# Optimization experiments

Measured on AMD Instinct MI355X. Metric: run time of the kernel, lower is better.

Reference implementation:

```python
import jax, jax.numpy as jnp
import numpy as np

HEADS = 8

def setup_inputs() -> dict:
    key = jax.random.key(0)
    ks = jax.random.split(key, 5)
    B, C, H, W = 2, 256, 64, 64
    dim = C
    x = jax.random.normal(ks[0], (B, C, H, W), dtype=jnp.float32)
    # Linear weights stored as [in, out] so y = x @ W + b
    w_qkv = jax.random.normal(ks[1], (dim, 3 * dim), dtype=jnp.float32) * (dim ** -0.5)
    b_qkv = jax.random.normal(ks[2], (3 * dim,), dtype=jnp.float32) * 0.02
    w_out = jax.random.normal(ks[3], (dim, dim), dtype=jnp.float32) * (dim ** -0.5)
    b_out = jax.random.normal(ks[4], (dim,), dtype=jnp.float32) * 0.02
    return {"x": x, "w_qkv": w_qkv, "b_qkv": b_qkv, "w_out": w_out, "b_out": b_out}

def reference(x, w_qkv, b_qkv, w_out, b_out):
    B, C, H, W = x.shape
    h = HEADS
    d = C // h
    scale = d ** -0.5
    # [B, C, H, W] -> [B, N, C]
    tokens = x.reshape(B, C, H * W).transpose(0, 2, 1)
    qkv = tokens @ w_qkv + b_qkv  # [B, N, 3C]
    q, k, v = jnp.split(qkv, 3, axis=-1)
    def to_heads(t):
        Bn, N, _ = t.shape
        return t.reshape(Bn, N, h, d).transpose(0, 2, 1, 3)  # [B, h, N, d]
    q, k, v = map(to_heads, (q, k, v))
    dots = jnp.einsum('bhnd,bhmd->bhnm', q, k) * scale  # [B, h, N, N]
    attn = jax.nn.softmax(dots, axis=-1)
    out = jnp.einsum('bhnm,bhmd->bhnd', attn, v)  # [B, h, N, d]
    out = out.transpose(0, 2, 1, 3).reshape(B, H * W, C)  # [B, N, C]
    out = out @ w_out + b_out
    return out.transpose(0, 2, 1).reshape(B, C, H, W)
```

## Files before the change

kernel.cpp:

```cpp
#include <hip/hip_runtime.h>

typedef __attribute__((ext_vector_type(8))) short s16x8;
typedef __attribute__((ext_vector_type(4))) short s16x4;
typedef __attribute__((ext_vector_type(4))) float f32x4;
typedef __attribute__((ext_vector_type(2))) unsigned u32x2;

#define MFMA32(a, b, c) __builtin_amdgcn_mfma_f32_16x16x32_bf16((a), (b), (c), 0, 0, 0)

#if __has_builtin(__builtin_amdgcn_mfma_f32_16x16x16bf16_1k)
#define MFMA16K(a, b, c) __builtin_amdgcn_mfma_f32_16x16x16bf16_1k((a), (b), (c), 0, 0, 0)
#else
#define MFMA16K(a, b, c) (c)
#endif

#if __has_builtin(__builtin_amdgcn_exp2f)
#define EXP2F(x) __builtin_amdgcn_exp2f(x)
#else
#define EXP2F(x) __exp2f(x)
#endif

#if __has_builtin(__builtin_amdgcn_rcpf)
#define RCPF(x) __builtin_amdgcn_rcpf(x)
#else
#define RCPF(x) (1.0f / (x))
#endif

#define SL2E 0.25507313f

__device__ __forceinline__ unsigned pkrne(float a, float b) {
  unsigned ua = __builtin_bit_cast(unsigned, a);
  unsigned ub = __builtin_bit_cast(unsigned, b);
  ua += 0x7FFFu + ((ua >> 16) & 1u);
  ub += 0x7FFFu + ((ub >> 16) & 1u);
  return __builtin_amdgcn_perm(ub, ua, 0x07060302u);
}

__device__ __forceinline__ unsigned pktrunc(float a, float b) {
  return __builtin_amdgcn_perm(__builtin_bit_cast(unsigned, b),
                               __builtin_bit_cast(unsigned, a), 0x07060302u);
}

__device__ __forceinline__ unsigned short bfr(float f) {
  unsigned u = __builtin_bit_cast(unsigned, f);
  u += 0x7FFFu + ((u >> 16) & 1u);
  return (unsigned short)(u >> 16);
}

__global__ __launch_bounds__(256) void prep_kernel(
    const float* __restrict__ x, const float* __restrict__ wqkv,
    const float* __restrict__ wout, ushort* __restrict__ xbf,
    ushort* __restrict__ wT, ushort* __restrict__ woT) {
  const int t = threadIdx.x;
  const int sub = t & 15, grp = t >> 4;
  const int id = blockIdx.x;
  const float* src;
  ushort* dst;
  int src_ld, k0, n0;
  float sc = 1.f;
  if (id < 512) {
    int mt = id & 63, kt = (id >> 6) & 3, b = id >> 8;
    src = x + (size_t)b * 256 * 4096;
    src_ld = 4096;
    dst = xbf + (size_t)b * 4096 * 256;
    k0 = kt * 64;
    n0 = mt * 64;
  } else if (id < 560) {
    int r = id - 512, nt = r % 12, kt = r / 12;
    src = wqkv;
    src_ld = 768;
    dst = wT;
    k0 = kt * 64;
    n0 = nt * 64;
    if (n0 < 256) sc = SL2E;
  } else {
    int r = id - 560, nt = r & 3, kt = r >> 2;
    src = wout;
    src_ld = 256;
    dst = woT;
    k0 = kt * 64;
    n0 = nt * 64;
  }
  const int k = k0 + grp * 4;
  const int n = n0 + sub * 4;
  unsigned d0[4], d1[4];
#pragma unroll
  for (int i = 0; i < 4; ++i) {
    float4 v = *(const float4*)(src + (size_t)(k + i) * src_ld + n);
    d0[i] = pkrne(v.x * sc, v.y * sc);
    d1[i] = pkrne(v.z * sc, v.w * sc);
  }
  u32x2 r0 = {__builtin_amdgcn_perm(d0[1], d0[0], 0x05040100u),
              __builtin_amdgcn_perm(d0[3], d0[2], 0x05040100u)};
  u32x2 r1 = {__builtin_amdgcn_perm(d0[1], d0[0], 0x07060302u),
              __builtin_amdgcn_perm(d0[3], d0[2], 0x07060302u)};
  u32x2 r2 = {__builtin_amdgcn_perm(d1[1], d1[0], 0x05040100u),
              __builtin_amdgcn_perm(d1[3], d1[2], 0x05040100u)};
  u32x2 r3 = {__builtin_amdgcn_perm(d1[1], d1[0], 0x07060302u),
              __builtin_amdgcn_perm(d1[3], d1[2], 0x07060302u)};
  *(u32x2*)(dst + (size_t)(n + 0) * 256 + k) = r0;
  *(u32x2*)(dst + (size_t)(n + 1) * 256 + k) = r1;
  *(u32x2*)(dst + (size_t)(n + 2) * 256 + k) = r2;
  *(u32x2*)(dst + (size_t)(n + 3) * 256 + k) = r3;
}

__global__ __launch_bounds__(256) void qkv_kernel(
    const ushort* __restrict__ xbf, const ushort* __restrict__ wT,
    const float* __restrict__ bq, ushort* __restrict__ QG,
    ushort* __restrict__ KG, ushort* __restrict__ VtG) {
  __shared__ __align__(16) ushort Wl[64][40];
  __shared__ __align__(16) ushort Xl[128][40];
  const int t0 = blockIdx.x * 128;
  const int n0 = blockIdx.y * 64;
  const int t = threadIdx.x;
  const int wid = t >> 6, lane = t & 63;
  const int wy = wid >> 1, wx = wid & 1;
  const int quad = lane >> 4, l16 = lane & 15;
  f32x4 acc[2][4] = {};
  const int wr = t >> 2, wsg = t & 3;
  for (int k0 = 0; k0 < 256; k0 += 32) {
    __syncthreads();
    *(uint4*)&Wl[wr][wsg * 8] =
        *(const uint4*)(wT + (size_t)(n0 + wr) * 256 + k0 + wsg * 8);
#pragma unroll
    for (int i = 0; i < 2; ++i) {
      int fid = t + 256 * i, row = fid >> 2, seg = fid & 3;
      *(uint4*)&Xl[row][seg * 8] =
          *(const uint4*)(xbf + (size_t)(t0 + row) * 256 + k0 + seg * 8);
    }
    __syncthreads();
    s16x8 wf[2], xf[4];
#pragma unroll
    for (int i = 0; i < 2; ++i)
      wf[i] = *(const s16x8*)&Wl[32 * wy + 16 * i + l16][quad * 8];
#pragma unroll
    for (int j = 0; j < 4; ++j)
      xf[j] = *(const s16x8*)&Xl[64 * wx + 16 * j + l16][quad * 8];
#pragma unroll
    for (int i = 0; i < 2; ++i)
#pragma unroll
      for (int j = 0; j < 4; ++j) acc[i][j] = MFMA32(wf[i], xf[j], acc[i][j]);
  }
  if (n0 < 512) {
    ushort* dst = (n0 < 256) ? QG : KG;
    const float bsc = (n0 < 256) ? SL2E : 1.f;
#pragma unroll
    for (int i = 0; i < 2; ++i) {
      int nb = n0 + 32 * wy + 16 * i + 4 * quad;
      float4 b4 = *(const float4*)(bq + nb);
      float bx0 = b4.x * bsc, bx1 = b4.y * bsc, bx2 = b4.z * bsc,
            bx3 = b4.w * bsc;
      int h = ((nb & 255) >> 5);
      int dd0 = nb & 31;
#pragma unroll
      for (int j = 0; j < 4; ++j) {
        int tok = t0 + 64 * wx + 16 * j + l16;
        int b = tok >> 12, tokn = tok & 4095;
        u32x2 pk = {pkrne(acc[i][j][0] + bx0, acc[i][j][1] + bx1),
                    pkrne(acc[i][j][2] + bx2, acc[i][j][3] + bx3)};
        *(u32x2*)(dst + ((size_t)(b * 8 + h) * 4096 + tokn) * 32 + dd0) = pk;
      }
    }
  } else {
#pragma unroll
    for (int i = 0; i < 2; ++i) {
      int nb = n0 + 32 * wy + 16 * i + 4 * quad;
      float4 b4 = *(const float4*)(bq + nb);
      float bb[4] = {b4.x, b4.y, b4.z, b4.w};
#pragma unroll
      for (int r = 0; r < 4; ++r) {
        int nn = nb + r - 512;
        int h = nn >> 5, ddv = nn & 31;
        ushort* vrow = VtG + (size_t)(h * 32 + ddv) * 4096;
#pragma unroll
        for (int j = 0; j < 4; ++j) {
          int tok = t0 + 64 * wx + 16 * j + l16;
          int b = tok >> 12, tokn = tok & 4095;
          vrow[(size_t)b * 8 * 32 * 4096 + tokn] = bfr(acc[i][j][r] + bb[r]);
        }
      }
    }
  }
}

__global__ __launch_bounds__(256) void attn_split(
    const ushort* __restrict__ QG, const ushort* __restrict__ KG,
    const ushort* __restrict__ VtG, float* __restrict__ OF,
    float* __restrict__ LF) {
  __shared__ __align__(16) ushort Kl[2][64][40];
  __shared__ __align__(16) ushort Vl[2][32][72];
  const int id = blockIdx.x;
  const int bh = (id & 7) * 2 + ((id >> 3) & 1);
  const int q0 = ((id >> 4) & 31) * 128;
  const int sp = id >> 9;
  const int kt0 = sp * 32, kt1 = kt0 + 32;
  const int t = threadIdx.x;
  const int wid = t >> 6, lane = t & 63;
  const int quad = lane >> 4, l16 = lane & 15;
  const size_t base = (size_t)bh * 4096 * 32;
  const ushort* qp = QG + base;
  const ushort* kp = KG + base;
  const ushort* vp = VtG + base;
  const int qw = q0 + 32 * wid;
  const s16x8 qf0 = *(const s16x8*)(qp + (size_t)(qw + l16) * 32 + quad * 8);
  const s16x8 qf1 = *(const s16x8*)(qp + (size_t)(qw + 16 + l16) * 32 + quad * 8);
  const int kr = t >> 2, ks = t & 3;
  const int vr = t >> 3, vsg = t & 7;
  *(uint4*)&Kl[0][kr][ks * 8] =
      *(const uint4*)(kp + (size_t)(kt0 * 64 + kr) * 32 + ks * 8);
  *(uint4*)&Vl[0][vr][vsg * 8] =
      *(const uint4*)(vp + (size_t)vr * 4096 + kt0 * 64 + vsg * 8);
  const ushort* kpre = kp + (size_t)((kt0 + 1) * 64 + kr) * 32 + ks * 8;
  const ushort* vpre = vp + (size_t)vr * 4096 + (kt0 + 1) * 64 + vsg * 8;
  __syncthreads();
  f32x4 o00 = {}, o01 = {}, o10 = {}, o11 = {}, ol0 = {}, ol1 = {};
  const f32x4 zero = {};
  const s16x4 ones = {(short)0x3F80, (short)0x3F80, (short)0x3F80,
                      (short)0x3F80};
#pragma unroll 2
  for (int kt = kt0; kt < kt1; ++kt) {
    const int cur = kt & 1;
    const bool more = (kt + 1) < kt1;
    uint4 kv, vv;
    if (more) {
      kv = *(const uint4*)kpre;
      vv = *(const uint4*)vpre;
      kpre += 2048;
      vpre += 64;
    }
    f32x4 st0[4], st1[4];
#pragma unroll
    for (int nb = 0; nb < 4; ++nb) {
      s16x8 kf = *(const s16x8*)&Kl[cur][16 * nb + l16][quad * 8];
      st0[nb] = MFMA32(kf, qf0, zero);
      st1[nb] = MFMA32(kf, qf1, zero);
    }
    unsigned pl0[4], ph0[4], pl1[4], ph1[4];
#pragma unroll
    for (int nb = 0; nb < 4; ++nb) {
      float a0 = EXP2F(st0[nb][0]);
      float a1 = EXP2F(st0[nb][1]);
      float a2 = EXP2F(st0[nb][2]);
      float a3 = EXP2F(st0[nb][3]);
      pl0[nb] = pktrunc(a0, a1);
      ph0[nb] = pktrunc(a2, a3);
      float b0 = EXP2F(st1[nb][0]);
      float b1 = EXP2F(st1[nb][1]);
      float b2 = EXP2F(st1[nb][2]);
      float b3 = EXP2F(st1[nb][3]);
      pl1[nb] = pktrunc(b0, b1);
      ph1[nb] = pktrunc(b2, b3);
    }
#pragma unroll
    for (int nb = 0; nb < 4; ++nb) {
      u32x2 pu0 = {pl0[nb], ph0[nb]};
      u32x2 pu1 = {pl1[nb], ph1[nb]};
      s16x4 pv0 = __builtin_bit_cast(s16x4, pu0);
      s16x4 pv1 = __builtin_bit_cast(s16x4, pu1);
      s16x4 va = *(const s16x4*)&Vl[cur][l16][16 * nb + quad * 4];
      s16x4 vb = *(const s16x4*)&Vl[cur][16 + l16][16 * nb + quad * 4];
      o00 = MFMA16K(va, pv0, o00);
      o01 = MFMA16K(vb, pv0, o01);
      o10 = MFMA16K(va, pv1, o10);
      o11 = MFMA16K(vb, pv1, o11);
      ol0 = MFMA16K(ones, pv0, ol0);
      ol1 = MFMA16K(ones, pv1, ol1);
    }
    if (more) {
      *(uint4*)&Kl[cur ^ 1][kr][ks * 8] = kv;
      *(uint4*)&Vl[cur ^ 1][vr][vsg * 8] = vv;
    }
    __syncthreads();
  }
  float* OFs = OF + (size_t)sp * 2097152;
  float* LFs = LF + (size_t)sp * 65536;
  const int tok0 = qw + l16;
  const size_t ob0 = ((size_t)bh * 4096 + tok0) * 32;
  const size_t ob1 = ob0 + (size_t)16 * 32;
  *(f32x4*)(OFs + ob0 + 4 * quad) = o00;
  *(f32x4*)(OFs + ob0 + 16 + 4 * quad) = o01;
  *(f32x4*)(OFs + ob1 + 4 * quad) = o10;
  *(f32x4*)(OFs + ob1 + 16 + 4 * quad) = o11;
  if (quad == 0) {
    LFs[(size_t)bh * 4096 + tok0] = ol0[0];
    LFs[(size_t)bh * 4096 + tok0 + 16] = ol1[0];
  }
}

__global__ __launch_bounds__(256) void proj_split(
    const float* __restrict__ OF, const float* __restrict__ LF,
    const ushort* __restrict__ woT, const float* __restrict__ bo,
    float* __restrict__ out) {
  __shared__ __align__(16) ushort Wl[64][40];
  __shared__ __align__(16) ushort Xl[128][40];
  const int t0 = blockIdx.x * 128;
  const int c0 = blockIdx.y * 64;
  const int t = threadIdx.x;
  const int wid = t >> 6, lane = t & 63;
  const int wy = wid >> 1, wx = wid & 1;
  const int quad = lane >> 4, l16 = lane & 15;
  f32x4 acc[2][4] = {};
  const int wr = t >> 2, wsg = t & 3;
  const int c8 = (t & 7) * 4;
  for (int k0 = 0; k0 < 256; k0 += 32) {
    __syncthreads();
    *(uint4*)&Wl[wr][wsg * 8] =
        *(const uint4*)(woT + (size_t)(c0 + wr) * 256 + k0 + wsg * 8);
    const int hh = k0 >> 5;
#pragma unroll
    for (int p = 0; p < 4; ++p) {
      int row = 32 * p + (t >> 3);
      int tok = t0 + row, bb = tok >> 12, tokn = tok & 4095;
      size_t ro = (size_t)(bb * 8 + hh) * 4096 + tokn;
      f32x4 v0 = *(const f32x4*)(OF + ro * 32 + c8);
      f32x4 v1 = *(const f32x4*)(OF + 2097152 + ro * 32 + c8);
      float l = LF[ro] + LF[65536 + ro];
      float inv = RCPF(l);
      f32x4 s = (v0 + v1) * inv;
      u32x2 pk = {pkrne(s[0], s[1]), pkrne(s[2], s[3])};
      *(u32x2*)&Xl[row][c8] = pk;
    }
    __syncthreads();
    s16x8 wf[2], xf[4];
#pragma unroll
    for (int i = 0; i < 2; ++i)
      wf[i] = *(const s16x8*)&Wl[32 * wy + 16 * i + l16][quad * 8];
#pragma unroll
    for (int j = 0; j < 4; ++j)
      xf[j] = *(const s16x8*)&Xl[64 * wx + 16 * j + l16][quad * 8];
#pragma unroll
    for (int i = 0; i < 2; ++i)
#pragma unroll
      for (int j = 0; j < 4; ++j) acc[i][j] = MFMA32(wf[i], xf[j], acc[i][j]);
  }
#pragma unroll
  for (int i = 0; i < 2; ++i) {
    int cb = c0 + 32 * wy + 16 * i + 4 * quad;
    float4 b4 = *(const float4*)(bo + cb);
    float bb[4] = {b4.x, b4.y, b4.z, b4.w};
#pragma unroll
    for (int j = 0; j < 4; ++j) {
      int tok = t0 + 64 * wx + 16 * j + l16;
      int b = tok >> 12, tokn = tok & 4095;
#pragma unroll
      for (int r = 0; r < 4; ++r)
        out[((size_t)(b * 256 + cb + r)) * 4096 + tokn] = acc[i][j][r] + bb[r];
    }
  }
}

__global__ __launch_bounds__(256) void attn_fb(
    const ushort* __restrict__ QG, const ushort* __restrict__ KG,
    const ushort* __restrict__ VtG, ushort* __restrict__ Ob) {
  __shared__ __align__(16) ushort Kl[2][64][40];
  __shared__ __align__(16) ushort Vl[2][32][72];
  const int id = blockIdx.x;
  const int bh = (id & 7) * 2 + ((id >> 3) & 1);
  const int q0 = (id >> 4) * 128;
  const int t = threadIdx.x;
  const int wid = t >> 6, lane = t & 63;
  const int quad = lane >> 4, l16 = lane & 15;
  const size_t base = (size_t)bh * 4096 * 32;
  const ushort* qp = QG + base;
  const ushort* kp = KG + base;
  const ushort* vp = VtG + base;
  const int qw = q0 + 32 * wid;
  const s16x8 qf0 = *(const s16x8*)(qp + (size_t)(qw + l16) * 32 + quad * 8);
  const s16x8 qf1 = *(const s16x8*)(qp + (size_t)(qw + 16 + l16) * 32 + quad * 8);
  const int kr = t >> 2, ks = t & 3;
  const int vr = t >> 3, vsg = t & 7;
  *(uint4*)&Kl[0][kr][ks * 8] = *(const uint4*)(kp + (size_t)kr * 32 + ks * 8);
  *(uint4*)&Vl[0][vr][vsg * 8] = *(const uint4*)(vp + (size_t)vr * 4096 + vsg * 8);
  const ushort* kpre = kp + (size_t)(64 + kr) * 32 + ks * 8;
  const ushort* vpre = vp + (size_t)vr * 4096 + 64 + vsg * 8;
  __syncthreads();
  f32x4 o00 = {}, o01 = {}, o10 = {}, o11 = {}, ol0 = {}, ol1 = {};
  const f32x4 zero = {};
  const s16x4 ones = {(short)0x3F80, (short)0x3F80, (short)0x3F80,
                      (short)0x3F80};
#pragma unroll 2
  for (int kt = 0; kt < 64; ++kt) {
    const int cur = kt & 1;
    const bool more = (kt + 1) < 64;
    uint4 kv, vv;
    if (more) {
      kv = *(const uint4*)kpre;
      vv = *(const uint4*)vpre;
      kpre += 2048;
      vpre += 64;
    }
    f32x4 st0[4], st1[4];
#pragma unroll
    for (int nb = 0; nb < 4; ++nb) {
      s16x8 kf = *(const s16x8*)&Kl[cur][16 * nb + l16][quad * 8];
      st0[nb] = MFMA32(kf, qf0, zero);
      st1[nb] = MFMA32(kf, qf1, zero);
    }
    unsigned pl0[4], ph0[4], pl1[4], ph1[4];
#pragma unroll
    for (int nb = 0; nb < 4; ++nb) {
      float a0 = EXP2F(st0[nb][0]);
      float a1 = EXP2F(st0[nb][1]);
      float a2 = EXP2F(st0[nb][2]);
      float a3 = EXP2F(st0[nb][3]);
      pl0[nb] = pktrunc(a0, a1);
      ph0[nb] = pktrunc(a2, a3);
      float b0 = EXP2F(st1[nb][0]);
      float b1 = EXP2F(st1[nb][1]);
      float b2 = EXP2F(st1[nb][2]);
      float b3 = EXP2F(st1[nb][3]);
      pl1[nb] = pktrunc(b0, b1);
      ph1[nb] = pktrunc(b2, b3);
    }
#pragma unroll
    for (int nb = 0; nb < 4; ++nb) {
      u32x2 pu0 = {pl0[nb], ph0[nb]};
      u32x2 pu1 = {pl1[nb], ph1[nb]};
      s16x4 pv0 = __builtin_bit_cast(s16x4, pu0);
      s16x4 pv1 = __builtin_bit_cast(s16x4, pu1);
      s16x4 va = *(const s16x4*)&Vl[cur][l16][16 * nb + quad * 4];
      s16x4 vb = *(const s16x4*)&Vl[cur][16 + l16][16 * nb + quad * 4];
      o00 = MFMA16K(va, pv0, o00);
      o01 = MFMA16K(vb, pv0, o01);
      o10 = MFMA16K(va, pv1, o10);
      o11 = MFMA16K(vb, pv1, o11);
      ol0 = MFMA16K(ones, pv0, ol0);
      ol1 = MFMA16K(ones, pv1, ol1);
    }
    if (more) {
      *(uint4*)&Kl[cur ^ 1][kr][ks * 8] = kv;
      *(uint4*)&Vl[cur ^ 1][vr][vsg * 8] = vv;
    }
    __syncthreads();
  }
  const float inv0 = 1.0f / ol0[0];
  const float inv1 = 1.0f / ol1[0];
  const int b = bh >> 3, h = bh & 7;
  const int tok0 = qw + l16;
  const size_t row0 = ((size_t)b * 4096 + tok0) * 256 + h * 32;
  const size_t row1 = row0 + (size_t)16 * 256;
  u32x2 w00 = {pkrne(o00[0] * inv0, o00[1] * inv0),
               pkrne(o00[2] * inv0, o00[3] * inv0)};
  u32x2 w01 = {pkrne(o01[0] * inv0, o01[1] * inv0),
               pkrne(o01[2] * inv0, o01[3] * inv0)};
  u32x2 w10 = {pkrne(o10[0] * inv1, o10[1] * inv1),
               pkrne(o10[2] * inv1, o10[3] * inv1)};
  u32x2 w11 = {pkrne(o11[0] * inv1, o11[1] * inv1),
               pkrne(o11[2] * inv1, o11[3] * inv1)};
  *(u32x2*)(Ob + row0 + 4 * quad) = w00;
  *(u32x2*)(Ob + row0 + 16 + 4 * quad) = w01;
  *(u32x2*)(Ob + row1 + 4 * quad) = w10;
  *(u32x2*)(Ob + row1 + 16 + 4 * quad) = w11;
}

__global__ __launch_bounds__(256) void proj_fb(
    const ushort* __restrict__ Ob, const ushort* __restrict__ woT,
    const float* __restrict__ bo, float* __restrict__ out) {
  __shared__ __align__(16) ushort Wl[64][40];
  __shared__ __align__(16) ushort Xl[128][40];
  const int t0 = blockIdx.x * 128;
  const int c0 = blockIdx.y * 64;
  const int t = threadIdx.x;
  const int wid = t >> 6, lane = t & 63;
  const int wy = wid >> 1, wx = wid & 1;
  const int quad = lane >> 4, l16 = lane & 15;
  f32x4 acc[2][4] = {};
  const int wr = t >> 2, wsg = t & 3;
  for (int k0 = 0; k0 < 256; k0 += 32) {
    __syncthreads();
    *(uint4*)&Wl[wr][wsg * 8] =
        *(const uint4*)(woT + (size_t)(c0 + wr) * 256 + k0 + wsg * 8);
#pragma unroll
    for (int i = 0; i < 2; ++i) {
      int fid = t + 256 * i, row = fid >> 2, seg = fid & 3;
      *(uint4*)&Xl[row][seg * 8] =
          *(const uint4*)(Ob + (size_t)(t0 + row) * 256 + k0 + seg * 8);
    }
    __syncthreads();
    s16x8 wf[2], xf[4];
#pragma unroll
    for (int i = 0; i < 2; ++i)
      wf[i] = *(const s16x8*)&Wl[32 * wy + 16 * i + l16][quad * 8];
#pragma unroll
    for (int j = 0; j < 4; ++j)
      xf[j] = *(const s16x8*)&Xl[64 * wx + 16 * j + l16][quad * 8];
#pragma unroll
    for (int i = 0; i < 2; ++i)
#pragma unroll
      for (int j = 0; j < 4; ++j) acc[i][j] = MFMA32(wf[i], xf[j], acc[i][j]);
  }
#pragma unroll
  for (int i = 0; i < 2; ++i) {
    int cb = c0 + 32 * wy + 16 * i + 4 * quad;
    float4 b4 = *(const float4*)(bo + cb);
    float bb[4] = {b4.x, b4.y, b4.z, b4.w};
#pragma unroll
    for (int j = 0; j < 4; ++j) {
      int tok = t0 + 64 * wx + 16 * j + l16;
      int b = tok >> 12, tokn = tok & 4095;
#pragma unroll
      for (int r = 0; r < 4; ++r)
        out[((size_t)(b * 256 + cb + r)) * 4096 + tokn] = acc[i][j][r] + bb[r];
    }
  }
}

extern "C" void kernel_launch(void* const* d_in, const int* in_sizes, int n_in,
                              void* d_out, int out_size, void* d_ws, size_t ws_size,
                              hipStream_t stream) {
  (void)in_sizes; (void)n_in; (void)out_size;
  const float* x = (const float*)d_in[0];
  const float* wq = (const float*)d_in[1];
  const float* bq = (const float*)d_in[2];
  const float* wo = (const float*)d_in[3];
  const float* bo = (const float*)d_in[4];
  float* out = (float*)d_out;
  ushort* ws = (ushort*)d_ws;
  ushort* xbf = ws;
  ushort* Ob  = ws;
  ushort* QG  = ws + 2097152;
  ushort* KG  = ws + 4194304;
  ushort* VtG = ws + 6291456;
  ushort* wT  = ws + 8388608;
  ushort* woT = ws + 8585216;
  float* OF = (float*)(ws + 8650752);
  float* LF = OF + 4194304;
  const bool split = ws_size >= 34603008;
  prep_kernel<<<576, 256, 0, stream>>>(x, wq, wo, xbf, wT, woT);
  qkv_kernel<<<dim3(64, 12), 256, 0, stream>>>(xbf, wT, bq, QG, KG, VtG);
  if (split) {
    attn_split<<<1024, 256, 0, stream>>>(QG, KG, VtG, OF, LF);
    proj_split<<<dim3(64, 4), 256, 0, stream>>>(OF, LF, woT, bo, out);
  } else {
    attn_fb<<<512, 256, 0, stream>>>(QG, KG, VtG, Ob);
    proj_fb<<<dim3(64, 4), 256, 0, stream>>>(Ob, woT, bo, out);
  }
}
```

Before: 144.0 us.

## Split attention KV range four ways and store partial outputs in bf16

The attention kernel now splits the key range into four chunks instead of two, doubling the grid to 2048 blocks, and adds a launch-bounds occupancy hint. Partial unnormalized outputs are packed to bf16 rather than stored as fp32, so the partial-output traffic stays moderate despite twice as many splits. The projection kernel sums four bf16 partials and four row sums before normalizing. This trades more partial reads and extra rounding error for more parallelism across CUs.

```diff
diff --git a/kernel.cpp b/kernel.cpp
--- a/kernel.cpp
+++ b/kernel.cpp
@@ -44,6 +44,13 @@
   unsigned u = __builtin_bit_cast(unsigned, f);
   u += 0x7FFFu + ((u >> 16) & 1u);
   return (unsigned short)(u >> 16);
+}
+
+__device__ __forceinline__ float bflo(unsigned u) {
+  return __builtin_bit_cast(float, u << 16);
+}
+__device__ __forceinline__ float bfhi(unsigned u) {
+  return __builtin_bit_cast(float, u & 0xFFFF0000u);
 }
 
 __global__ __launch_bounds__(256) void prep_kernel(
@@ -182,17 +189,17 @@
   }
 }
 
-__global__ __launch_bounds__(256) void attn_split(
+__global__ __launch_bounds__(256, 8) void attn_split(
     const ushort* __restrict__ QG, const ushort* __restrict__ KG,
-    const ushort* __restrict__ VtG, float* __restrict__ OF,
-    float* __restrict__ LF) {
+    const ushort* __restrict__ VtG, ushort* __restrict__ OF0,
+    ushort* __restrict__ OFb, float* __restrict__ LF) {
   __shared__ __align__(16) ushort Kl[2][64][40];
   __shared__ __align__(16) ushort Vl[2][32][72];
   const int id = blockIdx.x;
   const int bh = (id & 7) * 2 + ((id >> 3) & 1);
   const int q0 = ((id >> 4) & 31) * 128;
   const int sp = id >> 9;
-  const int kt0 = sp * 32, kt1 = kt0 + 32;
+  const int kt0 = sp * 16, kt1 = kt0 + 16;
   const int t = threadIdx.x;
   const int wid = t >> 6, lane = t & 63;
   const int quad = lane >> 4, l16 = lane & 15;
@@ -271,15 +278,19 @@
     }
     __syncthreads();
   }
-  float* OFs = OF + (size_t)sp * 2097152;
+  ushort* OFs = (sp == 0) ? OF0 : OFb + (size_t)(sp - 1) * 2097152;
   float* LFs = LF + (size_t)sp * 65536;
   const int tok0 = qw + l16;
   const size_t ob0 = ((size_t)bh * 4096 + tok0) * 32;
   const size_t ob1 = ob0 + (size_t)16 * 32;
-  *(f32x4*)(OFs + ob0 + 4 * quad) = o00;
-  *(f32x4*)(OFs + ob0 + 16 + 4 * quad) = o01;
-  *(f32x4*)(OFs + ob1 + 4 * quad) = o10;
-  *(f32x4*)(OFs + ob1 + 16 + 4 * quad) = o11;
+  u32x2 w00 = {pkrne(o00[0], o00[1]), pkrne(o00[2], o00[3])};
+  u32x2 w01 = {pkrne(o01[0], o01[1]), pkrne(o01[2], o01[3])};
+  u32x2 w10 = {pkrne(o10[0], o10[1]), pkrne(o10[2], o10[3])};
+  u32x2 w11 = {pkrne(o11[0], o11[1]), pkrne(o11[2], o11[3])};
+  *(u32x2*)(OFs + ob0 + 4 * quad) = w00;
+  *(u32x2*)(OFs + ob0 + 16 + 4 * quad) = w01;
+  *(u32x2*)(OFs + ob1 + 4 * quad) = w10;
+  *(u32x2*)(OFs + ob1 + 16 + 4 * quad) = w11;
   if (quad == 0) {
     LFs[(size_t)bh * 4096 + tok0] = ol0[0];
     LFs[(size_t)bh * 4096 + tok0 + 16] = ol1[0];
@@ -287,9 +298,9 @@
 }
 
 __global__ __launch_bounds__(256) void proj_split(
-    const float* __restrict__ OF, const float* __restrict__ LF,
-    const ushort* __restrict__ woT, const float* __restrict__ bo,
-    float* __restrict__ out) {
+    const ushort* __restrict__ OF0, const ushort* __restrict__ OFb,
+    const float* __restrict__ LF, const ushort* __restrict__ woT,
+    const float* __restrict__ bo, float* __restrict__ out) {
   __shared__ __align__(16) ushort Wl[64][40];
   __shared__ __align__(16) ushort Xl[128][40];
   const int t0 = blockIdx.x * 128;
@@ -311,11 +322,19 @@
       int row = 32 * p + (t >> 3);
       int tok = t0 + row, bb = tok >> 12, tokn = tok & 4095;
       size_t ro = (size_t)(bb * 8 + hh) * 4096 + tokn;
-      f32x4 v0 = *(const f32x4*)(OF + ro * 32 + c8);
-      f32x4 v1 = *(const f32x4*)(OF + 2097152 + ro * 32 + c8);
-      float l = LF[ro] + LF[65536 + ro];
+      size_t oi = ro * 32 + c8;
+      uint2 a0 = *(const uint2*)(OF0 + oi);
+      uint2 a1 = *(const uint2*)(OFb + oi);
+      uint2 a2 = *(const uint2*)(OFb + 2097152 + oi);
+      uint2 a3 = *(const uint2*)(OFb + 4194304 + oi);
+      float l = (LF[ro] + LF[65536 + ro]) + (LF[131072 + ro] + LF[196608 + ro]);
       float inv = RCPF(l);
-      f32x4 s = (v0 + v1) * inv;
+      f32x4 s;
+      s[0] = (bflo(a0.x) + bflo(a1.x)) + (bflo(a2.x) + bflo(a3.x));
+      s[1] = (bfhi(a0.x) + bfhi(a1.x)) + (bfhi(a2.x) + bfhi(a3.x));
+      s[2] = (bflo(a0.y) + bflo(a1.y)) + (bflo(a2.y) + bflo(a3.y));
+      s[3] = (bfhi(a0.y) + bfhi(a1.y)) + (bfhi(a2.y) + bfhi(a3.y));
+      s *= inv;
       u32x2 pk = {pkrne(s[0], s[1]), pkrne(s[2], s[3])};
       *(u32x2*)&Xl[row][c8] = pk;
     }
@@ -517,19 +536,20 @@
   ushort* ws = (ushort*)d_ws;
   ushort* xbf = ws;
   ushort* Ob  = ws;
+  ushort* OF0 = ws;
   ushort* QG  = ws + 2097152;
   ushort* KG  = ws + 4194304;
   ushort* VtG = ws + 6291456;
   ushort* wT  = ws + 8388608;
   ushort* woT = ws + 8585216;
-  float* OF = (float*)(ws + 8650752);
-  float* LF = OF + 4194304;
-  const bool split = ws_size >= 34603008;
+  ushort* OFb = ws + 8650752;
+  float* LF = (float*)(ws + 14942208);
+  const bool split = ws_size >= 30932992;
   prep_kernel<<<576, 256, 0, stream>>>(x, wq, wo, xbf, wT, woT);
   qkv_kernel<<<dim3(64, 12), 256, 0, stream>>>(xbf, wT, bq, QG, KG, VtG);
   if (split) {
-    attn_split<<<1024, 256, 0, stream>>>(QG, KG, VtG, OF, LF);
-    proj_split<<<dim3(64, 4), 256, 0, stream>>>(OF, LF, woT, bo, out);
+    attn_split<<<2048, 256, 0, stream>>>(QG, KG, VtG, OF0, OFb, LF);
+    proj_split<<<dim3(64, 4), 256, 0, stream>>>(OF0, OFb, LF, woT, bo, out);
   } else {
     attn_fb<<<512, 256, 0, stream>>>(QG, KG, VtG, Ob);
     proj_fb<<<dim3(64, 4), 256, 0, stream>>>(Ob, woT, bo, out);
```

New measurement: 287.8 us. 2x slower.
